# Performance work log

Hardware: AMD Instinct MI355X
Metric: run time of the kernel (lower is better)

The kernel has to match this reference:

```python
import jax, jax.numpy as jnp
import numpy as np

NUM_GRAPHS = 256   # number of graph blocks in the batch
NODES = 64         # nodes per graph (PPGN uses complete pair set per graph)
C_IN = 64          # nedgeinput
C_OUT = 64         # nedgeoutput
E = NUM_GRAPHS * NODES * NODES  # total pair-edges


def _complete_edge_index():
    # PPGN edge set: all (i, j) node pairs within each graph, sorted lexicographically
    base = np.arange(NUM_GRAPHS, dtype=np.int32) * NODES
    ii = np.repeat(np.arange(NODES, dtype=np.int32), NODES)
    jj = np.tile(np.arange(NODES, dtype=np.int32), NODES)
    src = (base[:, None] + ii[None, :]).reshape(-1)
    dst = (base[:, None] + jj[None, :]).reshape(-1)
    return jnp.asarray(np.stack([src, dst]), dtype=jnp.int32)  # [2, E]


def setup_inputs() -> dict:
    key = jax.random.key(0)
    k1, k2, k3, k4 = jax.random.split(key, 4)
    edge_index = _complete_edge_index()
    SP = jax.random.normal(k1, (E, C_IN), dtype=jnp.float32)
    s = 1.0 / np.sqrt(C_IN).astype(np.float32)
    W4 = jax.random.normal(k2, (C_IN, C_IN), dtype=jnp.float32) * s   # fc1_4.weight
    W5 = jax.random.normal(k3, (C_IN, C_IN), dtype=jnp.float32) * s   # fc1_5.weight
    W6 = jax.random.normal(k4, (C_OUT, 2 * C_IN), dtype=jnp.float32) * (1.0 / np.sqrt(2 * C_IN).astype(np.float32))  # fc1_6.weight
    return {"edge_index": edge_index, "SP": SP, "W4": W4, "W5": W5, "W6": W6}


def reference(edge_index, SP, W4, W5, W6):
    # X = fc1_4(SP)/C, Y = fc1_5(SP)/C  (torch Linear: x @ W.T)
    X = (SP @ W4.T) / C_IN   # [E, C]
    Y = (SP @ W5.T) / C_IN   # [E, C]
    # block-diagonal sparse matmul per channel, restricted back to the edge pattern
    g = edge_index[0] // NODES   # graph id per edge
    il = edge_index[0] % NODES   # local row index
    jl = edge_index[1] % NODES   # local col index
    Xd = jnp.zeros((NUM_GRAPHS, NODES, NODES, C_IN), X.dtype).at[g, il, jl].set(X)
    Yd = jnp.zeros((NUM_GRAPHS, NODES, NODES, C_IN), Y.dtype).at[g, il, jl].set(Y)
    prod = jnp.einsum('bikc,bkjc->bijc', Xd, Yd)  # per-graph, per-channel matmul X @ Y
    mm = prod[g, il, jl]                           # gather back to edge list: [E, C]
    tmp = jnp.concatenate([SP, mm], axis=1)        # [E, 2C]
    return jax.nn.relu(tmp @ W6.T)                 # [E, C_OUT]
```

## Files before the change

kernel.cpp:

```cpp
#include <hip/hip_runtime.h>
#include <stdint.h>

#define NG   256
#define NN   64
#define NEDGE (NG*NN*NN)

using bf8   = __attribute__((ext_vector_type(8))) short;
using f32x4 = __attribute__((ext_vector_type(4))) float;

__device__ __forceinline__ unsigned short f2bf(float f) {
  uint32_t u = __float_as_uint(f);
  u += 0x7fffu + ((u >> 16) & 1u);
  return (unsigned short)(u >> 16);
}
__device__ __forceinline__ bf8 pk8(float4 a, float4 b) {
  bf8 r;
  r[0]=(short)f2bf(a.x); r[1]=(short)f2bf(a.y); r[2]=(short)f2bf(a.z); r[3]=(short)f2bf(a.w);
  r[4]=(short)f2bf(b.x); r[5]=(short)f2bf(b.y); r[6]=(short)f2bf(b.z); r[7]=(short)f2bf(b.w);
  return r;
}
__device__ __forceinline__ bf8 ld8bf(const float* p) {
  const float4* q = reinterpret_cast<const float4*>(p);
  return pk8(q[0], q[1]);
}
__device__ __forceinline__ bf8 u4_to_bf8(uint4 v) {
  union { uint4 u; bf8 b; } c; c.u = v; return c.b;
}

__global__ __launch_bounds__(256) void k1_xy(
    const float* __restrict__ SP, const float* __restrict__ W4,
    const float* __restrict__ W5, unsigned short* __restrict__ Xp,
    unsigned short* __restrict__ Yp)
{
  __shared__ unsigned short Wl[2][64*72];
  __shared__ unsigned short lT[2][64*72];
  const int t = threadIdx.x, w = t >> 6, lane = t & 63;
  const int lr = lane & 15, lg = lane >> 4;
  const size_t b = blockIdx.x >> 4;
  const int i0 = ((int)blockIdx.x & 15) * 4;

  {
    const int mat = t >> 7, row = (t >> 1) & 63, h = t & 1;
    const float* src = (mat ? W5 : W4) + row*64 + h*32;
    unsigned short* dst = Wl[mat] + row*72 + h*32;
#pragma unroll
    for (int q = 0; q < 4; ++q) {
      bf8 v = ld8bf(src + q*8);
      *reinterpret_cast<bf8*>(dst + q*8) = v;
    }
  }

#define SPADDR(it_) (SP + ((size_t)b*4096 + (size_t)(i0+(it_))*64 + w*16 + lr)*64 + lg*8)
#define PRELOAD(P0_,P1_,P2_,P3_, it_)                                        \
  { const float4* q = reinterpret_cast<const float4*>(SPADDR(it_));          \
    P0_ = q[0]; P1_ = q[1]; P2_ = q[8]; P3_ = q[9]; }

  float4 pA0, pA1, pA2, pA3, pB0, pB1, pB2, pB3;
  PRELOAD(pA0,pA1,pA2,pA3, 0)
  PRELOAD(pB0,pB1,pB2,pB3, 1)
  __syncthreads();

#define WFRAG(mat_, ct_, kk_)                                                \
  (*reinterpret_cast<const bf8*>(Wl[mat_] + ((ct_)*16 + lr)*72 + (kk_)*32 + lg*8))

  const float s = 0.015625f;
#define K1_W1(arr_, ct_, r_, v_)                                             \
  lT[arr_][((ct_)*16 + lg*4 + (r_))*72 + w*16 + lr] = f2bf((v_)*s);
#define K1_W(ct_, ax_, ay_)                                                  \
  K1_W1(0,ct_,0,ax_[0]) K1_W1(0,ct_,1,ax_[1])                                \
  K1_W1(0,ct_,2,ax_[2]) K1_W1(0,ct_,3,ax_[3])                                \
  K1_W1(1,ct_,0,ay_[0]) K1_W1(1,ct_,1,ay_[1])                                \
  K1_W1(1,ct_,2,ay_[2]) K1_W1(1,ct_,3,ay_[3])

#define K1_ITER(it_, P0_,P1_,P2_,P3_, NEXT_)                                 \
  {                                                                          \
    bf8 a0 = pk8(P0_, P1_);                                                  \
    bf8 a1 = pk8(P2_, P3_);                                                  \
    NEXT_                                                                    \
    f32x4 ax0={0.f,0.f,0.f,0.f}, ax1=ax0, ax2=ax0, ax3=ax0;                  \
    f32x4 ay0=ax0, ay1=ax0, ay2=ax0, ay3=ax0;                                \
    ax0 = __builtin_amdgcn_mfma_f32_16x16x32_bf16(WFRAG(0,0,0), a0, ax0,0,0,0);\
    ax0 = __builtin_amdgcn_mfma_f32_16x16x32_bf16(WFRAG(0,0,1), a1, ax0,0,0,0);\
    ay0 = __builtin_amdgcn_mfma_f32_16x16x32_bf16(WFRAG(1,0,0), a0, ay0,0,0,0);\
    ay0 = __builtin_amdgcn_mfma_f32_16x16x32_bf16(WFRAG(1,0,1), a1, ay0,0,0,0);\
    ax1 = __builtin_amdgcn_mfma_f32_16x16x32_bf16(WFRAG(0,1,0), a0, ax1,0,0,0);\
    ax1 = __builtin_amdgcn_mfma_f32_16x16x32_bf16(WFRAG(0,1,1), a1, ax1,0,0,0);\
    ay1 = __builtin_amdgcn_mfma_f32_16x16x32_bf16(WFRAG(1,1,0), a0, ay1,0,0,0);\
    ay1 = __builtin_amdgcn_mfma_f32_16x16x32_bf16(WFRAG(1,1,1), a1, ay1,0,0,0);\
    ax2 = __builtin_amdgcn_mfma_f32_16x16x32_bf16(WFRAG(0,2,0), a0, ax2,0,0,0);\
    ax2 = __builtin_amdgcn_mfma_f32_16x16x32_bf16(WFRAG(0,2,1), a1, ax2,0,0,0);\
    ay2 = __builtin_amdgcn_mfma_f32_16x16x32_bf16(WFRAG(1,2,0), a0, ay2,0,0,0);\
    ay2 = __builtin_amdgcn_mfma_f32_16x16x32_bf16(WFRAG(1,2,1), a1, ay2,0,0,0);\
    ax3 = __builtin_amdgcn_mfma_f32_16x16x32_bf16(WFRAG(0,3,0), a0, ax3,0,0,0);\
    ax3 = __builtin_amdgcn_mfma_f32_16x16x32_bf16(WFRAG(0,3,1), a1, ax3,0,0,0);\
    ay3 = __builtin_amdgcn_mfma_f32_16x16x32_bf16(WFRAG(1,3,0), a0, ay3,0,0,0);\
    ay3 = __builtin_amdgcn_mfma_f32_16x16x32_bf16(WFRAG(1,3,1), a1, ay3,0,0,0);\
    K1_W(0, ax0, ay0) K1_W(1, ax1, ay1) K1_W(2, ax2, ay2) K1_W(3, ax3, ay3)  \
    __syncthreads();                                                         \
    {                                                                        \
      const int jo = t & 7, rid = t >> 3;                                    \
      const int irow8 = (i0 + (it_)) * 8;                                    \
      _Pragma("unroll")                                                      \
      for (int q = 0; q < 4; ++q) {                                          \
        int row = q*32 + rid;                                                \
        int a = row >> 6, ch = row & 63;                                     \
        const unsigned short* p = lT[a] + ch*72 + jo*8;                      \
        uint2 lo = *reinterpret_cast<const uint2*>(p);                       \
        uint2 hi = *reinterpret_cast<const uint2*>(p + 4);                   \
        uint4 v; v.x = lo.x; v.y = lo.y; v.z = hi.x; v.w = hi.y;             \
        uint4* G = reinterpret_cast<uint4*>(a ? Yp : Xp);                    \
        G[(b*64 + ch)*512 + irow8 + jo] = v;                                 \
      }                                                                      \
    }                                                                        \
    __syncthreads();                                                         \
  }

  K1_ITER(0, pA0,pA1,pA2,pA3, PRELOAD(pA0,pA1,pA2,pA3, 2))
  K1_ITER(1, pB0,pB1,pB2,pB3, PRELOAD(pB0,pB1,pB2,pB3, 3))
  K1_ITER(2, pA0,pA1,pA2,pA3, )
  K1_ITER(3, pB0,pB1,pB2,pB3, )
}

__global__ __launch_bounds__(256) void k2_mfma(
    const unsigned short* __restrict__ Xp, const unsigned short* __restrict__ Yp,
    unsigned short* __restrict__ mmp)
{
  __shared__ unsigned short Ys[2][64*68];
  __shared__ unsigned short Ds[2][64*68];
  const int t = threadIdx.x, w = t >> 6, lane = t & 63;
  const int lr = lane & 15, lg = lane >> 4;
  const int bid = ((int)blockIdx.x & 7) * 1024 + ((int)blockIdx.x >> 3);
  const int pw = w >> 1;
  const int mh = w & 1;
  const int plane = bid*2 + pw;

  {
    const uint4* Yg = reinterpret_cast<const uint4*>(Yp) + (size_t)plane*512;
    unsigned short* ys = Ys[pw];
    const int kk = lane >> 3, jo = lane & 7;
#pragma unroll
    for (int it = 0; it < 4; ++it) {
      int row = mh*32 + it*8 + kk;
      uint4 v = Yg[row*8 + jo];
      *reinterpret_cast<uint2*>(ys + row*68 + jo*8)     = make_uint2(v.x, v.y);
      *reinterpret_cast<uint2*>(ys + row*68 + jo*8 + 4) = make_uint2(v.z, v.w);
    }
  }
  __syncthreads();

  const unsigned short* ys = Ys[pw];
#define K2_BF(bv_, nt_, kt_)                                                 \
  bf8 bv_;                                                                   \
  bv_[0] = (short)ys[((kt_)*32 + lg*8 + 0)*68 + (nt_)*16 + lr];              \
  bv_[1] = (short)ys[((kt_)*32 + lg*8 + 1)*68 + (nt_)*16 + lr];              \
  bv_[2] = (short)ys[((kt_)*32 + lg*8 + 2)*68 + (nt_)*16 + lr];              \
  bv_[3] = (short)ys[((kt_)*32 + lg*8 + 3)*68 + (nt_)*16 + lr];              \
  bv_[4] = (short)ys[((kt_)*32 + lg*8 + 4)*68 + (nt_)*16 + lr];              \
  bv_[5] = (short)ys[((kt_)*32 + lg*8 + 5)*68 + (nt_)*16 + lr];              \
  bv_[6] = (short)ys[((kt_)*32 + lg*8 + 6)*68 + (nt_)*16 + lr];              \
  bv_[7] = (short)ys[((kt_)*32 + lg*8 + 7)*68 + (nt_)*16 + lr];
  K2_BF(b00, 0, 0) K2_BF(b01, 0, 1)
  K2_BF(b10, 1, 0) K2_BF(b11, 1, 1)
  K2_BF(b20, 2, 0) K2_BF(b21, 2, 1)
  K2_BF(b30, 3, 0) K2_BF(b31, 3, 1)

  const uint4* Xg = reinterpret_cast<const uint4*>(Xp) + (size_t)plane*512;
  f32x4 c00={0.f,0.f,0.f,0.f}, c01=c00, c02=c00, c03=c00;
  f32x4 c10=c00, c11=c00, c12=c00, c13=c00;
#define K2_MT(mt_, c0_, c1_, c2_, c3_)                                       \
  {                                                                          \
    int row = mh*32 + (mt_)*16 + lr;                                         \
    bf8 alo = u4_to_bf8(Xg[row*8 + lg]);                                     \
    bf8 ahi = u4_to_bf8(Xg[row*8 + 4 + lg]);                                 \
    c0_ = __builtin_amdgcn_mfma_f32_16x16x32_bf16(alo, b00, c0_, 0, 0, 0);   \
    c0_ = __builtin_amdgcn_mfma_f32_16x16x32_bf16(ahi, b01, c0_, 0, 0, 0);   \
    c1_ = __builtin_amdgcn_mfma_f32_16x16x32_bf16(alo, b10, c1_, 0, 0, 0);   \
    c1_ = __builtin_amdgcn_mfma_f32_16x16x32_bf16(ahi, b11, c1_, 0, 0, 0);   \
    c2_ = __builtin_amdgcn_mfma_f32_16x16x32_bf16(alo, b20, c2_, 0, 0, 0);   \
    c2_ = __builtin_amdgcn_mfma_f32_16x16x32_bf16(ahi, b21, c2_, 0, 0, 0);   \
    c3_ = __builtin_amdgcn_mfma_f32_16x16x32_bf16(alo, b30, c3_, 0, 0, 0);   \
    c3_ = __builtin_amdgcn_mfma_f32_16x16x32_bf16(ahi, b31, c3_, 0, 0, 0);   \
  }
  K2_MT(0, c00, c01, c02, c03)
  K2_MT(1, c10, c11, c12, c13)

  unsigned short* ds = Ds[pw];
#define K2_D1(mt_, nt_, r_, v_)                                              \
  ds[(mh*32 + (mt_)*16 + lg*4 + (r_))*68 + (nt_)*16 + lr] = f2bf(v_);
#define K2_D(mt_, nt_, c_)                                                   \
  K2_D1(mt_,nt_,0,c_[0]) K2_D1(mt_,nt_,1,c_[1])                              \
  K2_D1(mt_,nt_,2,c_[2]) K2_D1(mt_,nt_,3,c_[3])
  K2_D(0,0,c00) K2_D(0,1,c01) K2_D(0,2,c02) K2_D(0,3,c03)
  K2_D(1,0,c10) K2_D(1,1,c11) K2_D(1,2,c12) K2_D(1,3,c13)
  __syncthreads();

  {
    uint4* Mg = reinterpret_cast<uint4*>(mmp) + (size_t)plane*512;
    const unsigned short* dsr = Ds[pw];
    const int kk = lane >> 3, jo = lane & 7;
#pragma unroll
    for (int it = 0; it < 4; ++it) {
      int row = mh*32 + it*8 + kk;
      uint2 lo = *reinterpret_cast<const uint2*>(dsr + row*68 + jo*8);
      uint2 hi = *reinterpret_cast<const uint2*>(dsr + row*68 + jo*8 + 4);
      uint4 v; v.x = lo.x; v.y = lo.y; v.z = hi.x; v.w = hi.y;
      Mg[row*8 + jo] = v;
    }
  }
}

__global__ __launch_bounds__(256) void k3_out(
    const float* __restrict__ SP, const unsigned short* __restrict__ mmp,
    const float* __restrict__ W6, float* __restrict__ out)
{
  __shared__ unsigned short lw[64*140];
  __shared__ unsigned short lm[64*268];
  const int t = threadIdx.x, w = t >> 6, lane = t & 63;
  const int lr = lane & 15, lg = lane >> 4;
  const size_t b = blockIdx.x >> 4;
  const int i0 = ((int)blockIdx.x & 15) * 4;

  {
    const int row = t >> 2, seg = t & 3;
    const float* src = W6 + row*128 + seg*32;
    unsigned short* dst = lw + row*140 + seg*32;
#pragma unroll
    for (int q = 0; q < 4; ++q) {
      bf8 v = ld8bf(src + q*8);
      *reinterpret_cast<bf8*>(dst + q*8) = v;
    }
  }

  {
    const uint4* Mg = reinterpret_cast<const uint4*>(mmp);
    const int jo = t & 7, rid = t >> 3;
#pragma unroll
    for (int it = 0; it < 8; ++it) {
      int row = it*32 + rid;
      int c = row >> 2, di = row & 3;
      uint4 v = Mg[(b*64 + c)*512 + (size_t)(i0 + di)*8 + jo];
      unsigned short* p = lm + c*268 + di*64 + jo*8;
      *reinterpret_cast<uint2*>(p)     = make_uint2(v.x, v.y);
      *reinterpret_cast<uint2*>(p + 4) = make_uint2(v.z, v.w);
    }
  }

#define SP3ADDR(nt_) (SP + ((size_t)b*4096 + (size_t)(i0+w)*64 + (nt_)*16 + lr)*64 + lg*8)
#define PRELOAD3(P0_,P1_,P2_,P3_, nt_)                                       \
  { const float4* q = reinterpret_cast<const float4*>(SP3ADDR(nt_));         \
    P0_ = q[0]; P1_ = q[1]; P2_ = q[8]; P3_ = q[9]; }

  float4 pA0, pA1, pA2, pA3, pB0, pB1, pB2, pB3;
  PRELOAD3(pA0,pA1,pA2,pA3, 0)
  PRELOAD3(pB0,pB1,pB2,pB3, 1)
  __syncthreads();

#define W6F(ct_, kt_)                                                        \
  (*reinterpret_cast<const bf8*>(lw + ((ct_)*16 + lr)*140 + (kt_)*32 + lg*8))

#define K3_ITER(nt_, P0_,P1_,P2_,P3_, NEXT_)                                 \
  {                                                                          \
    bf8 a0 = pk8(P0_, P1_);                                                  \
    bf8 a1 = pk8(P2_, P3_);                                                  \
    NEXT_                                                                    \
    const int eloc = w*64 + (nt_)*16 + lr;                                   \
    const unsigned short* m2 = lm + (lg*8)*268 + eloc;                       \
    bf8 a2, a3;                                                              \
    a2[0]=(short)m2[0];      a2[1]=(short)m2[268];                           \
    a2[2]=(short)m2[536];    a2[3]=(short)m2[804];                           \
    a2[4]=(short)m2[1072];   a2[5]=(short)m2[1340];                          \
    a2[6]=(short)m2[1608];   a2[7]=(short)m2[1876];                          \
    const unsigned short* m3 = m2 + 32*268;                                  \
    a3[0]=(short)m3[0];      a3[1]=(short)m3[268];                           \
    a3[2]=(short)m3[536];    a3[3]=(short)m3[804];                           \
    a3[4]=(short)m3[1072];   a3[5]=(short)m3[1340];                          \
    a3[6]=(short)m3[1608];   a3[7]=(short)m3[1876];                          \
    f32x4 c0={0.f,0.f,0.f,0.f}, c1=c0, c2=c0, c3=c0;                         \
    c0 = __builtin_amdgcn_mfma_f32_16x16x32_bf16(W6F(0,0), a0, c0, 0,0,0);   \
    c0 = __builtin_amdgcn_mfma_f32_16x16x32_bf16(W6F(0,1), a1, c0, 0,0,0);   \
    c0 = __builtin_amdgcn_mfma_f32_16x16x32_bf16(W6F(0,2), a2, c0, 0,0,0);   \
    c0 = __builtin_amdgcn_mfma_f32_16x16x32_bf16(W6F(0,3), a3, c0, 0,0,0);   \
    c1 = __builtin_amdgcn_mfma_f32_16x16x32_bf16(W6F(1,0), a0, c1, 0,0,0);   \
    c1 = __builtin_amdgcn_mfma_f32_16x16x32_bf16(W6F(1,1), a1, c1, 0,0,0);   \
    c1 = __builtin_amdgcn_mfma_f32_16x16x32_bf16(W6F(1,2), a2, c1, 0,0,0);   \
    c1 = __builtin_amdgcn_mfma_f32_16x16x32_bf16(W6F(1,3), a3, c1, 0,0,0);   \
    c2 = __builtin_amdgcn_mfma_f32_16x16x32_bf16(W6F(2,0), a0, c2, 0,0,0);   \
    c2 = __builtin_amdgcn_mfma_f32_16x16x32_bf16(W6F(2,1), a1, c2, 0,0,0);   \
    c2 = __builtin_amdgcn_mfma_f32_16x16x32_bf16(W6F(2,2), a2, c2, 0,0,0);   \
    c2 = __builtin_amdgcn_mfma_f32_16x16x32_bf16(W6F(2,3), a3, c2, 0,0,0);   \
    c3 = __builtin_amdgcn_mfma_f32_16x16x32_bf16(W6F(3,0), a0, c3, 0,0,0);   \
    c3 = __builtin_amdgcn_mfma_f32_16x16x32_bf16(W6F(3,1), a1, c3, 0,0,0);   \
    c3 = __builtin_amdgcn_mfma_f32_16x16x32_bf16(W6F(3,2), a2, c3, 0,0,0);   \
    c3 = __builtin_amdgcn_mfma_f32_16x16x32_bf16(W6F(3,3), a3, c3, 0,0,0);   \
    const size_t e = b*4096 + (size_t)(i0 + w)*64 + (nt_)*16 + lr;           \
    float* ob = out + e*64 + lg*4;                                           \
    f32x4 o;                                                                 \
    o[0]=fmaxf(c0[0],0.f); o[1]=fmaxf(c0[1],0.f);                            \
    o[2]=fmaxf(c0[2],0.f); o[3]=fmaxf(c0[3],0.f);                            \
    *reinterpret_cast<f32x4*>(ob) = o;                                       \
    o[0]=fmaxf(c1[0],0.f); o[1]=fmaxf(c1[1],0.f);                            \
    o[2]=fmaxf(c1[2],0.f); o[3]=fmaxf(c1[3],0.f);                            \
    *reinterpret_cast<f32x4*>(ob + 16) = o;                                  \
    o[0]=fmaxf(c2[0],0.f); o[1]=fmaxf(c2[1],0.f);                            \
    o[2]=fmaxf(c2[2],0.f); o[3]=fmaxf(c2[3],0.f);                            \
    *reinterpret_cast<f32x4*>(ob + 32) = o;                                  \
    o[0]=fmaxf(c3[0],0.f); o[1]=fmaxf(c3[1],0.f);                            \
    o[2]=fmaxf(c3[2],0.f); o[3]=fmaxf(c3[3],0.f);                            \
    *reinterpret_cast<f32x4*>(ob + 48) = o;                                  \
  }

  K3_ITER(0, pA0,pA1,pA2,pA3, PRELOAD3(pA0,pA1,pA2,pA3, 2))
  K3_ITER(1, pB0,pB1,pB2,pB3, PRELOAD3(pB0,pB1,pB2,pB3, 3))
  K3_ITER(2, pA0,pA1,pA2,pA3, )
  K3_ITER(3, pB0,pB1,pB2,pB3, )
}

extern "C" void kernel_launch(void* const* d_in, const int* in_sizes, int n_in,
                              void* d_out, int out_size, void* d_ws, size_t ws_size,
                              hipStream_t stream)
{
  (void)in_sizes; (void)n_in; (void)out_size; (void)ws_size;
  const float* SP = (const float*)d_in[1];
  const float* W4 = (const float*)d_in[2];
  const float* W5 = (const float*)d_in[3];
  const float* W6 = (const float*)d_in[4];

  unsigned short* Xp = (unsigned short*)d_out;
  unsigned short* Yp = Xp + (size_t)NEDGE * 64;
  unsigned short* mmp = (unsigned short*)d_ws;
  float* out = (float*)d_out;

  k1_xy  <<<NG*16,    256, 0, stream>>>(SP, W4, W5, Xp, Yp);
  k2_mfma<<<NG*32,    256, 0, stream>>>(Xp, Yp, mmp);
  k3_out <<<NG*16,    256, 0, stream>>>(SP, mmp, W6, out);
}
```

Measured before the change: 328.7 us.

## Store mm in edge-major tiled layout so k3 reads it directly without LDS

k2 now writes the per-graph product in a layout grouped by (graph, row, column-group) with channels interleaved, instead of channel-planar. k3 then loads its MFMA operand fragments straight from global memory into registers, with prefetch alongside the SP loads. This removes the LDS staging buffer and its transpose in k3, which cuts LDS use and may raise occupancy. The cost is that k2 stores become more scattered and k3 issues many 2-byte strided global loads.

Measured after the change: 341.3 us. 3.9% more time.

```diff
diff --git a/kernel.cpp b/kernel.cpp
--- a/kernel.cpp
+++ b/kernel.cpp
@@ -123,7 +123,7 @@
 
 __global__ __launch_bounds__(256) void k2_mfma(
     const unsigned short* __restrict__ Xp, const unsigned short* __restrict__ Yp,
-    unsigned short* __restrict__ mmp)
+    unsigned short* __restrict__ mmh)
 {
   __shared__ unsigned short Ys[2][64*68];
   __shared__ unsigned short Ds[2][64*68];
@@ -195,26 +195,26 @@
   __syncthreads();
 
   {
-    uint4* Mg = reinterpret_cast<uint4*>(mmp) + (size_t)plane*512;
+    uint4* Mg = reinterpret_cast<uint4*>(mmh);
     const unsigned short* dsr = Ds[pw];
     const int kk = lane >> 3, jo = lane & 7;
+    const int bb = plane >> 6, cc = plane & 63;
 #pragma unroll
     for (int it = 0; it < 4; ++it) {
       int row = mh*32 + it*8 + kk;
       uint2 lo = *reinterpret_cast<const uint2*>(dsr + row*68 + jo*8);
       uint2 hi = *reinterpret_cast<const uint2*>(dsr + row*68 + jo*8 + 4);
       uint4 v; v.x = lo.x; v.y = lo.y; v.z = hi.x; v.w = hi.y;
-      Mg[row*8 + jo] = v;
+      Mg[((size_t)bb*256 + row*4 + (jo>>1))*128 + cc*2 + (jo&1)] = v;
     }
   }
 }
 
 __global__ __launch_bounds__(256) void k3_out(
-    const float* __restrict__ SP, const unsigned short* __restrict__ mmp,
+    const float* __restrict__ SP, const unsigned short* __restrict__ mmh,
     const float* __restrict__ W6, float* __restrict__ out)
 {
   __shared__ unsigned short lw[64*140];
-  __shared__ unsigned short lm[64*268];
   const int t = threadIdx.x, w = t >> 6, lane = t & 63;
   const int lr = lane & 15, lg = lane >> 4;
   const size_t b = blockIdx.x >> 4;
@@ -231,50 +231,42 @@
     }
   }
 
-  {
-    const uint4* Mg = reinterpret_cast<const uint4*>(mmp);
-    const int jo = t & 7, rid = t >> 3;
-#pragma unroll
-    for (int it = 0; it < 8; ++it) {
-      int row = it*32 + rid;
-      int c = row >> 2, di = row & 3;
-      uint4 v = Mg[(b*64 + c)*512 + (size_t)(i0 + di)*8 + jo];
-      unsigned short* p = lm + c*268 + di*64 + jo*8;
-      *reinterpret_cast<uint2*>(p)     = make_uint2(v.x, v.y);
-      *reinterpret_cast<uint2*>(p + 4) = make_uint2(v.z, v.w);
-    }
-  }
-
 #define SP3ADDR(nt_) (SP + ((size_t)b*4096 + (size_t)(i0+w)*64 + (nt_)*16 + lr)*64 + lg*8)
 #define PRELOAD3(P0_,P1_,P2_,P3_, nt_)                                       \
   { const float4* q = reinterpret_cast<const float4*>(SP3ADDR(nt_));         \
     P0_ = q[0]; P1_ = q[1]; P2_ = q[8]; P3_ = q[9]; }
 
+  const unsigned short* mmb =
+      mmh + ((size_t)b*256 + (size_t)(i0 + w)*4)*1024 + lg*128 + lr;
+#define MMLOAD(m2_, m3_, nt_)                                                \
+  { const unsigned short* tp = mmb + (nt_)*1024;                             \
+    m2_[0]=(short)tp[0];    m2_[1]=(short)tp[16];                            \
+    m2_[2]=(short)tp[32];   m2_[3]=(short)tp[48];                            \
+    m2_[4]=(short)tp[64];   m2_[5]=(short)tp[80];                            \
+    m2_[6]=(short)tp[96];   m2_[7]=(short)tp[112];                           \
+    m3_[0]=(short)tp[512];  m3_[1]=(short)tp[528];                           \
+    m3_[2]=(short)tp[544];  m3_[3]=(short)tp[560];                           \
+    m3_[4]=(short)tp[576];  m3_[5]=(short)tp[592];                           \
+    m3_[6]=(short)tp[608];  m3_[7]=(short)tp[624]; }
+
   float4 pA0, pA1, pA2, pA3, pB0, pB1, pB2, pB3;
+  bf8 m2A, m3A, m2B, m3B;
   PRELOAD3(pA0,pA1,pA2,pA3, 0)
   PRELOAD3(pB0,pB1,pB2,pB3, 1)
+  MMLOAD(m2A, m3A, 0)
+  MMLOAD(m2B, m3B, 1)
   __syncthreads();
 
 #define W6F(ct_, kt_)                                                        \
   (*reinterpret_cast<const bf8*>(lw + ((ct_)*16 + lr)*140 + (kt_)*32 + lg*8))
 
-#define K3_ITER(nt_, P0_,P1_,P2_,P3_, NEXT_)                                 \
+#define K3_ITER(nt_, P0_,P1_,P2_,P3_, M2_, M3_, NEXT_)                       \
   {                                                                          \
     bf8 a0 = pk8(P0_, P1_);                                                  \
     bf8 a1 = pk8(P2_, P3_);                                                  \
+    bf8 a2 = M2_;                                                            \
+    bf8 a3 = M3_;                                                            \
     NEXT_                                                                    \
-    const int eloc = w*64 + (nt_)*16 + lr;                                   \
-    const unsigned short* m2 = lm + (lg*8)*268 + eloc;                       \
-    bf8 a2, a3;                                                              \
-    a2[0]=(short)m2[0];      a2[1]=(short)m2[268];                           \
-    a2[2]=(short)m2[536];    a2[3]=(short)m2[804];                           \
-    a2[4]=(short)m2[1072];   a2[5]=(short)m2[1340];                          \
-    a2[6]=(short)m2[1608];   a2[7]=(short)m2[1876];                          \
-    const unsigned short* m3 = m2 + 32*268;                                  \
-    a3[0]=(short)m3[0];      a3[1]=(short)m3[268];                           \
-    a3[2]=(short)m3[536];    a3[3]=(short)m3[804];                           \
-    a3[4]=(short)m3[1072];   a3[5]=(short)m3[1340];                          \
-    a3[6]=(short)m3[1608];   a3[7]=(short)m3[1876];                          \
     f32x4 c0={0.f,0.f,0.f,0.f}, c1=c0, c2=c0, c3=c0;                         \
     c0 = __builtin_amdgcn_mfma_f32_16x16x32_bf16(W6F(0,0), a0, c0, 0,0,0);   \
     c0 = __builtin_amdgcn_mfma_f32_16x16x32_bf16(W6F(0,1), a1, c0, 0,0,0);   \
@@ -309,10 +301,12 @@
     *reinterpret_cast<f32x4*>(ob + 48) = o;                                  \
   }
 
-  K3_ITER(0, pA0,pA1,pA2,pA3, PRELOAD3(pA0,pA1,pA2,pA3, 2))
-  K3_ITER(1, pB0,pB1,pB2,pB3, PRELOAD3(pB0,pB1,pB2,pB3, 3))
-  K3_ITER(2, pA0,pA1,pA2,pA3, )
-  K3_ITER(3, pB0,pB1,pB2,pB3, )
+  K3_ITER(0, pA0,pA1,pA2,pA3, m2A, m3A,
+          PRELOAD3(pA0,pA1,pA2,pA3, 2) MMLOAD(m2A, m3A, 2))
+  K3_ITER(1, pB0,pB1,pB2,pB3, m2B, m3B,
+          PRELOAD3(pB0,pB1,pB2,pB3, 3) MMLOAD(m2B, m3B, 3))
+  K3_ITER(2, pA0,pA1,pA2,pA3, m2A, m3A, )
+  K3_ITER(3, pB0,pB1,pB2,pB3, m2B, m3B, )
 }
 
 extern "C" void kernel_launch(void* const* d_in, const int* in_sizes, int n_in,
@@ -327,10 +321,10 @@
 
   unsigned short* Xp = (unsigned short*)d_out;
   unsigned short* Yp = Xp + (size_t)NEDGE * 64;
-  unsigned short* mmp = (unsigned short*)d_ws;
+  unsigned short* mmh = (unsigned short*)d_ws;
   float* out = (float*)d_out;
 
   k1_xy  <<<NG*16,    256, 0, stream>>>(SP, W4, W5, Xp, Yp);
-  k2_mfma<<<NG*32,    256, 0, stream>>>(Xp, Yp, mmp);
-  k3_out <<<NG*16,    256, 0, stream>>>(SP, mmp, W6, out);
-}
+  k2_mfma<<<NG*32,    256, 0, stream>>>(Xp, Yp, mmh);
+  k3_out <<<NG*16,    256, 0, stream>>>(SP, mmh, W6, out);
+}
```
